# Kernel optimization log

Measured on AMD Instinct MI355X. Metric: run time of the kernel, lower is better.

The kernel has to match this reference:

```python
import jax, jax.numpy as jnp
import numpy as np

L = 4096
B = 8192

def setup_inputs() -> dict:
    key = jax.random.key(0)
    k1, k2 = jax.random.split(key)
    X = jax.random.normal(k1, (B, L), dtype=jnp.float32)
    # lengths in [1, L] so every row has at least one valid element
    N = jax.random.randint(k2, (B, 1), 1, L + 1, dtype=jnp.int32)
    return {"X": X, "N": N}

def reference(X, N):
    # mask[i, j] = j < N[i, 0]
    mask = (jnp.arange(X.shape[1])[None, :] < N).astype(X.dtype)  # [B, L]
    neg_inf = jnp.array(-jnp.inf, dtype=X.dtype)
    # row max over valid entries only
    max_X = jnp.max(jnp.where(mask > 0, X, neg_inf), axis=1, keepdims=True)  # [B, 1]
    exp_X = jnp.exp(X - max_X)  # computed over all entries, as in original
    sum_exp_X = jnp.sum(exp_X * mask, axis=1, keepdims=True)  # [B, 1]
    return mask * exp_X / sum_exp_X
```

## Files before the change

### kernel.cpp

```cpp
#include <hip/hip_runtime.h>
#include <math.h>

#define ROW_LEN 4096
#define NROWS   8192
#define BLOCK   256
#define WAVES_PER_BLOCK (BLOCK / 64)
#define F4_PER_LANE 16

typedef float vf4 __attribute__((ext_vector_type(4)));

__global__ __launch_bounds__(BLOCK) void masked_softmax_wave(
    const float* __restrict__ X,
    const int* __restrict__ N,
    float* __restrict__ out)
{
    const int wave = threadIdx.x >> 6;
    const int lane = threadIdx.x & 63;
    const int row  = blockIdx.x * WAVES_PER_BLOCK + wave;

    const int n = __builtin_amdgcn_readfirstlane(N[row]);

    const vf4* __restrict__ Xr = (const vf4*)(X + (size_t)row * ROW_LEN);
    vf4* __restrict__ Or       = (vf4*)(out + (size_t)row * ROW_LEN);

    vf4 v[F4_PER_LANE];
    const vf4 z4 = {0.0f, 0.0f, 0.0f, 0.0f};

    #pragma unroll
    for (int j = 0; j < F4_PER_LANE; j++) {
        v[j] = z4;
        if (256 * j < n) {
            if (4 * (lane + 64 * j) < n)
                v[j] = __builtin_nontemporal_load(&Xr[lane + 64 * j]);
        }
    }

    float m = -INFINITY;
    #pragma unroll
    for (int j = 0; j < F4_PER_LANE; j++) {
        if (256 * (j + 1) <= n) {
            m = fmaxf(m, fmaxf(fmaxf(v[j].x, v[j].y), fmaxf(v[j].z, v[j].w)));
        } else if (256 * j < n) {
            const int col = 4 * (lane + 64 * j);
            m = fmaxf(m, (col + 0 < n) ? v[j].x : -INFINITY);
            m = fmaxf(m, (col + 1 < n) ? v[j].y : -INFINITY);
            m = fmaxf(m, (col + 2 < n) ? v[j].z : -INFINITY);
            m = fmaxf(m, (col + 3 < n) ? v[j].w : -INFINITY);
        }
    }
    #pragma unroll
    for (int off = 1; off < 64; off <<= 1)
        m = fmaxf(m, __shfl_xor(m, off, 64));

    float s = 0.0f;
    #pragma unroll
    for (int j = 0; j < F4_PER_LANE; j++) {
        if (256 * (j + 1) <= n) {
            float ex = __expf(v[j].x - m);
            float ey = __expf(v[j].y - m);
            float ez = __expf(v[j].z - m);
            float ew = __expf(v[j].w - m);
            v[j].x = ex; v[j].y = ey; v[j].z = ez; v[j].w = ew;
            s += (ex + ey) + (ez + ew);
        } else if (256 * j < n) {
            const int col = 4 * (lane + 64 * j);
            float ex = __expf(v[j].x - m);
            float ey = __expf(v[j].y - m);
            float ez = __expf(v[j].z - m);
            float ew = __expf(v[j].w - m);
            ex = (col + 0 < n) ? ex : 0.0f;
            ey = (col + 1 < n) ? ey : 0.0f;
            ez = (col + 2 < n) ? ez : 0.0f;
            ew = (col + 3 < n) ? ew : 0.0f;
            v[j].x = ex; v[j].y = ey; v[j].z = ez; v[j].w = ew;
            s += (ex + ey) + (ez + ew);
        }
    }
    #pragma unroll
    for (int off = 1; off < 64; off <<= 1)
        s += __shfl_xor(s, off, 64);

    const float inv = 1.0f / s;

    #pragma unroll
    for (int j = 0; j < F4_PER_LANE; j++) {
        vf4 o = z4;
        if (256 * j < n) {
            o.x = v[j].x * inv;
            o.y = v[j].y * inv;
            o.z = v[j].z * inv;
            o.w = v[j].w * inv;
        }
        __builtin_nontemporal_store(o, &Or[lane + 64 * j]);
    }
}

extern "C" void kernel_launch(void* const* d_in, const int* in_sizes, int n_in,
                              void* d_out, int out_size, void* d_ws, size_t ws_size,
                              hipStream_t stream) {
    const float* X = (const float*)d_in[0];
    const int*   N = (const int*)d_in[1];
    float* out = (float*)d_out;
    masked_softmax_wave<<<NROWS / WAVES_PER_BLOCK, BLOCK, 0, stream>>>(X, N, out);
}
```

Baseline: 215.4 us.

## Process each row with a full block instead of a single wave

Switches from one wave per row (four rows per block) to one 256-thread block per row, with each thread holding four float4 values instead of sixteen. Row max and sum are combined across the four waves through shared memory and block barriers. This lowers per-thread register use, which should raise occupancy and memory-level parallelism, and gives all waves in a block the same row length. The cost is two barriers and LDS traffic per row.

```diff
diff --git a/kernel.cpp b/kernel.cpp
--- a/kernel.cpp
+++ b/kernel.cpp
@@ -4,24 +4,28 @@
 #define ROW_LEN 4096
 #define NROWS   8192
 #define BLOCK   256
-#define WAVES_PER_BLOCK (BLOCK / 64)
-#define F4_PER_LANE 16
+#define NWAVES  (BLOCK / 64)
+#define F4_PER_LANE 4
 
 typedef float vf4 __attribute__((ext_vector_type(4)));
 
-__global__ __launch_bounds__(BLOCK) void masked_softmax_wave(
+__global__ __launch_bounds__(BLOCK) void masked_softmax_block(
     const float* __restrict__ X,
     const int* __restrict__ N,
     float* __restrict__ out)
 {
-    const int wave = threadIdx.x >> 6;
-    const int lane = threadIdx.x & 63;
-    const int row  = blockIdx.x * WAVES_PER_BLOCK + wave;
+    const int tid  = threadIdx.x;
+    const int wave = tid >> 6;
+    const int lane = tid & 63;
+    const int row  = blockIdx.x;
 
     const int n = __builtin_amdgcn_readfirstlane(N[row]);
 
     const vf4* __restrict__ Xr = (const vf4*)(X + (size_t)row * ROW_LEN);
     vf4* __restrict__ Or       = (vf4*)(out + (size_t)row * ROW_LEN);
+
+    __shared__ float redm[NWAVES];
+    __shared__ float reds[NWAVES];
 
     vf4 v[F4_PER_LANE];
     const vf4 z4 = {0.0f, 0.0f, 0.0f, 0.0f};
@@ -29,19 +33,19 @@
     #pragma unroll
     for (int j = 0; j < F4_PER_LANE; j++) {
         v[j] = z4;
-        if (256 * j < n) {
-            if (4 * (lane + 64 * j) < n)
-                v[j] = __builtin_nontemporal_load(&Xr[lane + 64 * j]);
+        if (1024 * j < n) {
+            if (4 * (tid + 256 * j) < n)
+                v[j] = __builtin_nontemporal_load(&Xr[tid + 256 * j]);
         }
     }
 
     float m = -INFINITY;
     #pragma unroll
     for (int j = 0; j < F4_PER_LANE; j++) {
-        if (256 * (j + 1) <= n) {
+        if (1024 * (j + 1) <= n) {
             m = fmaxf(m, fmaxf(fmaxf(v[j].x, v[j].y), fmaxf(v[j].z, v[j].w)));
-        } else if (256 * j < n) {
-            const int col = 4 * (lane + 64 * j);
+        } else if (1024 * j < n) {
+            const int col = 4 * (tid + 256 * j);
             m = fmaxf(m, (col + 0 < n) ? v[j].x : -INFINITY);
             m = fmaxf(m, (col + 1 < n) ? v[j].y : -INFINITY);
             m = fmaxf(m, (col + 2 < n) ? v[j].z : -INFINITY);
@@ -51,19 +55,22 @@
     #pragma unroll
     for (int off = 1; off < 64; off <<= 1)
         m = fmaxf(m, __shfl_xor(m, off, 64));
+    if (lane == 0) redm[wave] = m;
+    __syncthreads();
+    m = fmaxf(fmaxf(redm[0], redm[1]), fmaxf(redm[2], redm[3]));
 
     float s = 0.0f;
     #pragma unroll
     for (int j = 0; j < F4_PER_LANE; j++) {
-        if (256 * (j + 1) <= n) {
+        if (1024 * (j + 1) <= n) {
             float ex = __expf(v[j].x - m);
             float ey = __expf(v[j].y - m);
             float ez = __expf(v[j].z - m);
             float ew = __expf(v[j].w - m);
             v[j].x = ex; v[j].y = ey; v[j].z = ez; v[j].w = ew;
             s += (ex + ey) + (ez + ew);
-        } else if (256 * j < n) {
-            const int col = 4 * (lane + 64 * j);
+        } else if (1024 * j < n) {
+            const int col = 4 * (tid + 256 * j);
             float ex = __expf(v[j].x - m);
             float ey = __expf(v[j].y - m);
             float ez = __expf(v[j].z - m);
@@ -79,19 +86,22 @@
     #pragma unroll
     for (int off = 1; off < 64; off <<= 1)
         s += __shfl_xor(s, off, 64);
+    if (lane == 0) reds[wave] = s;
+    __syncthreads();
+    s = (reds[0] + reds[1]) + (reds[2] + reds[3]);
 
     const float inv = 1.0f / s;
 
     #pragma unroll
     for (int j = 0; j < F4_PER_LANE; j++) {
         vf4 o = z4;
-        if (256 * j < n) {
+        if (1024 * j < n) {
             o.x = v[j].x * inv;
             o.y = v[j].y * inv;
             o.z = v[j].z * inv;
             o.w = v[j].w * inv;
         }
-        __builtin_nontemporal_store(o, &Or[lane + 64 * j]);
+        __builtin_nontemporal_store(o, &Or[tid + 256 * j]);
     }
 }
 
@@ -101,5 +111,5 @@
     const float* X = (const float*)d_in[0];
     const int*   N = (const int*)d_in[1];
     float* out = (float*)d_out;
-    masked_softmax_wave<<<NROWS / WAVES_PER_BLOCK, BLOCK, 0, stream>>>(X, N, out);
+    masked_softmax_block<<<NROWS, BLOCK, 0, stream>>>(X, N, out);
 }
```

After: 213.3 us. Within noise of the previous version (-1.0%).
